# Performance work log

Hardware: AMD Instinct MI355X
Metric: run time of the kernel (lower is better)

Reference implementation:

```python
import jax, jax.numpy as jnp
import numpy as np

B, T, M, K = 8, 128, 8, 16
EMBED, HID = 64, 128
KR = K + 1
N = M * KR
NEG_SLOPE = 0.2


def build_edges(num_instruments, k_with_root):
    edges = []
    Kr = k_with_root
    for m in range(num_instruments):
        base = m * Kr
        root = base + (Kr - 1)
        for kp in range(Kr - 1):
            edges.append((base + kp, root))
            edges.append((root, base + kp))
    roots = [m * Kr + (Kr - 1) for m in range(num_instruments)]
    for i in range(len(roots)):
        for j in range(i + 1, len(roots)):
            edges.append((roots[i], roots[j]))
            edges.append((roots[j], roots[i]))
    e = np.asarray(edges, dtype=np.int32)
    return jnp.asarray(e[:, 0]), jnp.asarray(e[:, 1])


def setup_inputs() -> dict:
    key = jax.random.key(0)
    ks = jax.random.split(key, 12)
    feat = jax.random.uniform(ks[0], (B, T, M, K, 3), dtype=jnp.float32)
    sc = 0.05
    W1 = jax.random.normal(ks[1], (3, EMBED), jnp.float32) * sc
    b1 = jnp.zeros((EMBED,), jnp.float32)
    W2 = jax.random.normal(ks[2], (EMBED, EMBED), jnp.float32) * sc
    b2 = jnp.zeros((EMBED,), jnp.float32)
    W_ih = jax.random.normal(ks[3], (4 * HID, EMBED), jnp.float32) * sc
    W_hh = jax.random.normal(ks[4], (4 * HID, HID), jnp.float32) * sc
    b_ih = jnp.zeros((4 * HID,), jnp.float32)
    b_hh = jnp.zeros((4 * HID,), jnp.float32)
    Wg = jax.random.normal(ks[5], (HID, HID), jnp.float32) * sc
    a_src = jax.random.normal(ks[6], (HID,), jnp.float32) * sc
    a_dst = jax.random.normal(ks[7], (HID,), jnp.float32) * sc
    src, dst = build_edges(M, KR)
    return {"feat": feat, "W1": W1, "b1": b1, "W2": W2, "b2": b2,
            "W_ih": W_ih, "W_hh": W_hh, "b_ih": b_ih, "b_hh": b_hh,
            "Wg": Wg, "a_src": a_src, "a_dst": a_dst, "src": src, "dst": dst}


def reference(feat, W1, b1, W2, b2, W_ih, W_hh, b_ih, b_hh, Wg, a_src, a_dst, src, dst):
    # --- add_virtual_root: (B,T,M,K,3) -> (B,T,M,K+1,3) ---
    xy = feat[..., :2]
    vis = feat[..., 2] > 0.5
    w = vis[..., None].astype(feat.dtype)
    denom = jnp.clip(jnp.sum(w, axis=3, keepdims=True), 1.0, None)
    root_xy = jnp.sum(xy * w, axis=3, keepdims=True) / denom
    root_vis = jnp.any(vis, axis=3, keepdims=True).astype(feat.dtype)[..., None]
    root_feat = jnp.concatenate([root_xy, root_vis], axis=-1)
    featR = jnp.concatenate([feat, root_feat], axis=3)  # (B,T,M,KR,3)
    b, t, m, kr, _ = featR.shape
    n = m * kr
    # --- phi MLP ---
    v = jnp.maximum(featR @ W1 + b1, 0.0) @ W2 + b2  # (B,T,M,KR,E)
    v = v.reshape(b, t, n, -1)
    # --- LSTM over time, batch = B*N (torch gate order i,f,g,o) ---
    x = v.transpose(1, 0, 2, 3).reshape(t, b * n, -1)  # (T, B*N, E)
    hdim = W_hh.shape[1]
    h0 = jnp.zeros((b * n, hdim), feat.dtype)
    def step(carry, xt):
        h, c = carry
        z = xt @ W_ih.T + b_ih + h @ W_hh.T + b_hh
        i, f, g, o = jnp.split(z, 4, axis=-1)
        c = jax.nn.sigmoid(f) * c + jax.nn.sigmoid(i) * jnp.tanh(g)
        h = jax.nn.sigmoid(o) * jnp.tanh(c)
        return (h, c), h
    _, hs = jax.lax.scan(step, (h0, h0), x)  # (T, B*N, H)
    r = hs.reshape(t, b, n, hdim).transpose(1, 0, 2, 3)  # (B,T,N,H)
    # --- GAT applied to all timesteps at once (fixed edge_index) ---
    h = r @ Wg                           # (B,T,N,H)
    s_src = h @ a_src                    # (B,T,N)
    s_dst = h @ a_dst
    e = s_src[:, :, src] + s_dst[:, :, dst]           # (B,T,E)
    e = jnp.where(e > 0, e, NEG_SLOPE * e)            # LeakyReLU(0.2)
    eT = e.transpose(2, 0, 1)                          # (E,B,T)
    mmax = jax.ops.segment_max(eT, dst, num_segments=n)  # (N,B,T)
    ex = jnp.exp(eT - mmax[dst])
    den = jax.ops.segment_sum(ex, dst, num_segments=n)   # (N,B,T)
    alpha = ex / den[dst]                               # (E,B,T)
    hT = h.transpose(2, 0, 1, 3)                        # (N,B,T,H)
    agg = jax.ops.segment_sum(alpha[..., None] * hT[src], dst, num_segments=n)
    rhat = jax.nn.elu(agg).transpose(1, 2, 0, 3)        # (B,T,N,H)
    return (r, rhat)
```

## Files before the change

### kernel.cpp

```cpp
#include <hip/hip_runtime.h>

#define TB 128
#define BB 8
#define MM 8
#define KP 16
#define KR 17
#define NN 136
#define EMB 64
#define HID 128
#define G4 512
#define BN 1088
#define NEG_SLOPE 0.2f

typedef _Float16 h4 __attribute__((ext_vector_type(4)));
typedef _Float16 h8 __attribute__((ext_vector_type(8)));
typedef float    f4v __attribute__((ext_vector_type(4)));

__device__ __forceinline__ float sigf(float x) { return 1.0f/(1.0f + __expf(-x)); }
__device__ __forceinline__ float tanhf_fast(float x) {
  x = fminf(fmaxf(x, -15.0f), 15.0f);
  float e = __expf(2.0f*x);
  return (e - 1.0f)/(e + 1.0f);
}
__device__ __forceinline__ void bar_lds() {
  asm volatile("s_waitcnt lgkmcnt(0)\n\ts_barrier" ::: "memory");
}

__global__ __launch_bounds__(256) void k1_mlp(
    const float* __restrict__ feat, const float* __restrict__ W1,
    const float* __restrict__ b1, const float* __restrict__ W2,
    const float* __restrict__ b2, float* __restrict__ x)
{
  __shared__ float fl[MM*KP*3];
  __shared__ float fR[NN][3];
  __shared__ float hidl[NN][EMB];
  const int bt = blockIdx.x;
  const int b = bt >> 7;
  const int t = bt & 127;
  const int tid = threadIdx.x;

  const float* fp = feat + (size_t)bt * (MM*KP*3);
  for (int i = tid; i < MM*KP*3; i += 256) fl[i] = fp[i];
  __syncthreads();

  if (tid < NN) {
    int n = tid, m = n / KR, kk = n - m*KR;
    if (kk < KP) {
      fR[n][0] = fl[(m*KP+kk)*3+0];
      fR[n][1] = fl[(m*KP+kk)*3+1];
      fR[n][2] = fl[(m*KP+kk)*3+2];
    } else {
      float sx = 0.f, sy = 0.f, sw = 0.f;
      for (int k = 0; k < KP; ++k) {
        float vz = fl[(m*KP+k)*3+2];
        float w = (vz > 0.5f) ? 1.0f : 0.0f;
        sx += fl[(m*KP+k)*3+0]*w;
        sy += fl[(m*KP+k)*3+1]*w;
        sw += w;
      }
      float dn = fmaxf(sw, 1.0f);
      fR[n][0] = sx/dn; fR[n][1] = sy/dn; fR[n][2] = (sw > 0.f) ? 1.f : 0.f;
    }
  }
  __syncthreads();

  const int p = tid & 31, e0 = p*2, nb = tid >> 5;
  float w10a = W1[e0],   w11a = W1[EMB+e0],   w12a = W1[2*EMB+e0],   b1a = b1[e0];
  float w10b = W1[e0+1], w11b = W1[EMB+e0+1], w12b = W1[2*EMB+e0+1], b1b = b1[e0+1];
  for (int ni = 0; ni < 17; ++ni) {
    int n = nb*17 + ni;
    float xx = fR[n][0], yy = fR[n][1], zz = fR[n][2];
    float va = fmaf(xx,w10a, fmaf(yy,w11a, fmaf(zz,w12a, b1a)));
    float vb = fmaf(xx,w10b, fmaf(yy,w11b, fmaf(zz,w12b, b1b)));
    *(float2*)&hidl[n][e0] = make_float2(fmaxf(va,0.f), fmaxf(vb,0.f));
  }
  float2 w2c[EMB];
  #pragma unroll
  for (int j = 0; j < EMB; ++j) w2c[j] = *(const float2*)&W2[(size_t)j*EMB + e0];
  float b2a = b2[e0], b2b = b2[e0+1];
  __syncthreads();

  float* xo = x + ((size_t)t*BN + (size_t)b*NN)*EMB + e0;
  for (int ni = 0; ni < 17; ++ni) {
    int n = nb*17 + ni;
    float aa = b2a, ab = b2b;
    const float4* h4p = (const float4*)hidl[n];
    #pragma unroll
    for (int j4 = 0; j4 < 16; ++j4) {
      float4 hv = h4p[j4];
      aa = fmaf(hv.x, w2c[4*j4+0].x, aa); ab = fmaf(hv.x, w2c[4*j4+0].y, ab);
      aa = fmaf(hv.y, w2c[4*j4+1].x, aa); ab = fmaf(hv.y, w2c[4*j4+1].y, ab);
      aa = fmaf(hv.z, w2c[4*j4+2].x, aa); ab = fmaf(hv.z, w2c[4*j4+2].y, ab);
      aa = fmaf(hv.w, w2c[4*j4+3].x, aa); ab = fmaf(hv.w, w2c[4*j4+3].y, ab);
    }
    *(float2*)&xo[(size_t)n*EMB] = make_float2(aa, ab);
  }
}

__global__ __launch_bounds__(512, 2) void k2_lstm(
    const float* __restrict__ x, const float* __restrict__ W_ih,
    const float* __restrict__ W_hh, const float* __restrict__ b_ih,
    const float* __restrict__ b_hh, float* __restrict__ r)
{
  __shared__ h8  Bh8[6*64];
  __shared__ h8  Bl8[6*64];
  __shared__ f4v zlds[32*64];
  const int tid = threadIdx.x;
  const int w   = tid >> 6;
  const int l   = tid & 63;
  const int lr  = l & 15;
  const int lg  = l >> 4;
  const int s0  = blockIdx.x * 16;

  h8 A[4][6];
  #pragma unroll
  for (int m = 0; m < 4; ++m) {
    int row = 64*w + 16*m + lr;
    const float* wih = W_ih + (size_t)row*64;
    const float* whh = W_hh + (size_t)row*128;
    #pragma unroll
    for (int kt = 0; kt < 6; ++kt) {
      int k = kt*32 + lg*8;
      float4 wv0 = (k < 64) ? *(const float4*)(wih + k)
                            : *(const float4*)(whh + (k - 64));
      float4 wv1 = (k+4 < 64) ? *(const float4*)(wih + k + 4)
                              : *(const float4*)(whh + (k + 4 - 64));
      A[m][kt] = h8{(_Float16)wv0.x,(_Float16)wv0.y,(_Float16)wv0.z,(_Float16)wv0.w,
                    (_Float16)wv1.x,(_Float16)wv1.y,(_Float16)wv1.z,(_Float16)wv1.w};
    }
  }
  #pragma unroll
  for (int m = 0; m < 4; ++m)
    #pragma unroll
    for (int kt = 0; kt < 6; ++kt)
      asm volatile("" : "+v"(A[m][kt]));

  f4v biasC[4];
  #pragma unroll
  for (int m = 0; m < 4; ++m)
    #pragma unroll
    for (int q = 0; q < 4; ++q) {
      int row = 64*w + 16*m + lg*4 + q;
      biasC[m][q] = b_ih[row] + b_hh[row];
    }

  const int j0 = 16*w + 4*lg;
  const int l2    = lr + 16*(2*(w&1) + (lg>>1));
  const int halfB = lg & 1;
  const int hIdx  = (2 + (w>>1))*64 + l2;
  const int xIdx  = (w>>1)*64 + l2;

  const int qq = s0 + lr;
  const int b  = qq / NN, n = qq - b*NN;
  float* rp0 = r + (((size_t)b*TB)*NN + n)*HID + j0;
  const size_t rstep = (size_t)NN*HID;

  {
    h4 z0 = h4{(_Float16)0.f,(_Float16)0.f,(_Float16)0.f,(_Float16)0.f};
    ((h4*)Bh8)[256 + tid] = z0;
    ((h4*)Bl8)[256 + tid] = z0;
    if (w < 4) {
      float4 xv = *(const float4*)(x + ((size_t)(s0 + lr))*EMB + 16*w + 4*lg);
      h4 xh = h4{(_Float16)xv.x,(_Float16)xv.y,(_Float16)xv.z,(_Float16)xv.w};
      h4 xl = h4{(_Float16)(xv.x-(float)xh[0]),(_Float16)(xv.y-(float)xh[1]),
                 (_Float16)(xv.z-(float)xh[2]),(_Float16)(xv.w-(float)xh[3])};
      ((h4*)&Bh8[xIdx])[halfB] = xh;
      ((h4*)&Bl8[xIdx])[halfB] = xl;
    }
  }
  __syncthreads();

  float c0=0.f, c1=0.f, c2=0.f, c3=0.f;

  for (int t = 0; t < TB; ++t) {
    float4 xpre = make_float4(0.f,0.f,0.f,0.f);
    if (w < 4) {
      int tp = (t+1 < TB) ? t+1 : t;
      xpre = *(const float4*)(x + ((size_t)tp*BN + s0 + lr)*EMB + 16*w + 4*lg);
    }

    f4v C[4] = {biasC[0], biasC[1], biasC[2], biasC[3]};
    #pragma unroll
    for (int kt = 0; kt < 6; ++kt) {
      h8 bh = Bh8[kt*64 + l];
      h8 bl = Bl8[kt*64 + l];
      #pragma unroll
      for (int m = 0; m < 4; ++m)
        C[m] = __builtin_amdgcn_mfma_f32_16x16x32_f16(A[m][kt], bh, C[m], 0, 0, 0);
      #pragma unroll
      for (int m = 0; m < 4; ++m)
        C[m] = __builtin_amdgcn_mfma_f32_16x16x32_f16(A[m][kt], bl, C[m], 0, 0, 0);
    }
    #pragma unroll
    for (int m = 0; m < 4; ++m) zlds[(4*w + m)*64 + l] = C[m];
    bar_lds();

    f4v zi = zlds[(0*8 + w)*64 + l];
    f4v zf = zlds[(1*8 + w)*64 + l];
    f4v zg = zlds[(2*8 + w)*64 + l];
    f4v zo = zlds[(3*8 + w)*64 + l];
    float h0,h1,h2,h3;
    { float cc = sigf(zf[0])*c0 + sigf(zi[0])*tanhf_fast(zg[0]); h0 = sigf(zo[0])*tanhf_fast(cc); c0 = cc; }
    { float cc = sigf(zf[1])*c1 + sigf(zi[1])*tanhf_fast(zg[1]); h1 = sigf(zo[1])*tanhf_fast(cc); c1 = cc; }
    { float cc = sigf(zf[2])*c2 + sigf(zi[2])*tanhf_fast(zg[2]); h2 = sigf(zo[2])*tanhf_fast(cc); c2 = cc; }
    { float cc = sigf(zf[3])*c3 + sigf(zi[3])*tanhf_fast(zg[3]); h3 = sigf(zo[3])*tanhf_fast(cc); c3 = cc; }
    *(float4*)(rp0 + (size_t)t*rstep) = make_float4(h0,h1,h2,h3);
    h4 hh = h4{(_Float16)h0,(_Float16)h1,(_Float16)h2,(_Float16)h3};
    h4 hl = h4{(_Float16)(h0-(float)hh[0]),(_Float16)(h1-(float)hh[1]),
               (_Float16)(h2-(float)hh[2]),(_Float16)(h3-(float)hh[3])};
    ((h4*)&Bh8[hIdx])[halfB] = hh;
    ((h4*)&Bl8[hIdx])[halfB] = hl;
    if (w < 4) {
      h4 xh = h4{(_Float16)xpre.x,(_Float16)xpre.y,(_Float16)xpre.z,(_Float16)xpre.w};
      h4 xl = h4{(_Float16)(xpre.x-(float)xh[0]),(_Float16)(xpre.y-(float)xh[1]),
                 (_Float16)(xpre.z-(float)xh[2]),(_Float16)(xpre.w-(float)xh[3])};
      ((h4*)&Bh8[xIdx])[halfB] = xh;
      ((h4*)&Bl8[xIdx])[halfB] = xl;
    }
    bar_lds();
  }
}

__global__ __launch_bounds__(256) void k3_gat(
    const float* __restrict__ r, const float* __restrict__ Wg,
    const float* __restrict__ a_src, const float* __restrict__ a_dst,
    float* __restrict__ rhat)
{
  __shared__ float rl[NN*132];
  __shared__ float waS[HID], waD[HID];
  __shared__ float ssrc[NN], sdst[NN];
  __shared__ float alpha[MM][24];
  __shared__ float aggR[MM][HID];
  __shared__ float v16[HID*20];
  __shared__ float h2[16][HID];
  const int bt = blockIdx.x;
  const int tid = threadIdx.x;
  const float* rb = r + (size_t)bt*NN*HID;

  {
    const float4* rb4 = (const float4*)rb;
    for (int i = tid; i < NN*32; i += 256) {
      int n = i >> 5, k4 = i & 31;
      *(float4*)&rl[n*132 + k4*4] = rb4[i];
    }
  }
  {
    int half = tid >> 7, j = tid & 127;
    const float* av = half ? a_dst : a_src;
    float acc = 0.f;
    for (int k = 0; k < HID; ++k) acc = fmaf(Wg[(size_t)k*HID + j], av[k], acc);
    if (half) waD[j] = acc; else waS[j] = acc;
  }
  __syncthreads();
  for (int job = tid; job < 2*NN; job += 256) {
    int n = job >> 1, which = job & 1;
    const float4* rn = (const float4*)&rl[n*132];
    const float4* wa = (const float4*)(which ? waD : waS);
    float acc = 0.f;
    #pragma unroll
    for (int i = 0; i < 32; ++i) {
      float4 a4 = rn[i], b4 = wa[i];
      acc = fmaf(a4.x,b4.x, fmaf(a4.y,b4.y, fmaf(a4.z,b4.z, fmaf(a4.w,b4.w, acc))));
    }
    if (which) sdst[n] = acc; else ssrc[n] = acc;
  }
  __syncthreads();
  if (tid < MM) {
    int m = tid;
    float sd = sdst[m*KR + KP];
    float ev[23]; float mx = -1e30f;
    #pragma unroll
    for (int k = 0; k < 23; ++k) {
      int srcn;
      if (k < KP) srcn = m*KR + k;
      else { int rr = k - KP; rr += (rr >= m) ? 1 : 0; srcn = rr*KR + KP; }
      float e = ssrc[srcn] + sd;
      e = (e > 0.f) ? e : NEG_SLOPE*e;
      ev[k] = e; mx = fmaxf(mx, e);
    }
    float den = 0.f;
    #pragma unroll
    for (int k = 0; k < 23; ++k) { float ex = __expf(ev[k]-mx); ev[k] = ex; den += ex; }
    float inv = 1.f/den;
    #pragma unroll
    for (int k = 0; k < 23; ++k) alpha[m][k] = ev[k]*inv;
  }
  __syncthreads();
  {
    int m = tid >> 5, jq = (tid & 31)*4;
    float4 acc = make_float4(0.f,0.f,0.f,0.f);
    #pragma unroll
    for (int k = 0; k < 23; ++k) {
      int srcn;
      if (k < KP) srcn = m*KR + k;
      else { int rr = k - KP; rr += (rr >= m) ? 1 : 0; srcn = rr*KR + KP; }
      float al = alpha[m][k];
      float4 hv = *(const float4*)&rl[srcn*132 + jq];
      acc.x = fmaf(al, hv.x, acc.x); acc.y = fmaf(al, hv.y, acc.y);
      acc.z = fmaf(al, hv.z, acc.z); acc.w = fmaf(al, hv.w, acc.w);
    }
    *(float4*)&aggR[m][jq] = acc;
  }
  __syncthreads();
  for (int idx = tid; idx < 16*HID; idx += 256) {
    int k = idx & 127, row = idx >> 7;
    float v = (row < 8) ? rl[(row*KR + KP)*132 + k] : aggR[row-8][k];
    v16[k*20 + row] = v;
  }
  __syncthreads();
  {
    int half = tid >> 7, j = tid & 127;
    float acc[8] = {0.f,0.f,0.f,0.f,0.f,0.f,0.f,0.f};
    const float* wgp = Wg + j;
    #pragma unroll 4
    for (int k = 0; k < HID; ++k) {
      float wv = wgp[(size_t)k*HID];
      const float4* vv = (const float4*)&v16[k*20 + half*8];
      float4 va = vv[0], vb = vv[1];
      acc[0] = fmaf(va.x, wv, acc[0]); acc[1] = fmaf(va.y, wv, acc[1]);
      acc[2] = fmaf(va.z, wv, acc[2]); acc[3] = fmaf(va.w, wv, acc[3]);
      acc[4] = fmaf(vb.x, wv, acc[4]); acc[5] = fmaf(vb.y, wv, acc[5]);
      acc[6] = fmaf(vb.z, wv, acc[6]); acc[7] = fmaf(vb.w, wv, acc[7]);
    }
    #pragma unroll
    for (int q = 0; q < 8; ++q) h2[half*8 + q][j] = acc[q];
  }
  __syncthreads();
  {
    int j = tid & 127, half = tid >> 7;
    float* out = rhat + (size_t)bt*NN*HID + j;
    for (int ni = 0; ni < 68; ++ni) {
      int n = half*68 + ni;
      int m = n / KR, kk = n - m*KR;
      float v = (kk < KP) ? h2[m][j] : h2[8+m][j];
      v = (v > 0.f) ? v : (__expf(v) - 1.f);
      out[(size_t)n*HID] = v;
    }
  }
}

extern "C" void kernel_launch(void* const* d_in, const int* in_sizes, int n_in,
                              void* d_out, int out_size, void* d_ws, size_t ws_size,
                              hipStream_t stream) {
  (void)in_sizes; (void)n_in; (void)out_size; (void)ws_size;
  const float* feat  = (const float*)d_in[0];
  const float* W1    = (const float*)d_in[1];
  const float* b1    = (const float*)d_in[2];
  const float* W2    = (const float*)d_in[3];
  const float* b2    = (const float*)d_in[4];
  const float* W_ih  = (const float*)d_in[5];
  const float* W_hh  = (const float*)d_in[6];
  const float* b_ih  = (const float*)d_in[7];
  const float* b_hh  = (const float*)d_in[8];
  const float* Wg    = (const float*)d_in[9];
  const float* a_src = (const float*)d_in[10];
  const float* a_dst = (const float*)d_in[11];

  float* x    = (float*)d_ws;
  float* r    = (float*)d_out;
  float* rhat = r + (size_t)BB*TB*NN*HID;

  k1_mlp<<<BB*TB, 256, 0, stream>>>(feat, W1, b1, W2, b2, x);
  k2_lstm<<<68, 512, 0, stream>>>(x, W_ih, W_hh, b_ih, b_hh, r);
  k3_gat<<<BB*TB, 256, 0, stream>>>(r, Wg, a_src, a_dst, rhat);
}
```

Measured before the change: 607.7 us.

## Remap LSTM gate rows per wave and precompute next-step input projection

Each wave now owns matching rows of all four gates (i,f,g,o) for its 16 hidden units. The z staging buffer in LDS and one of the two barriers per timestep are gone, since the gate math reads the MFMA accumulators directly. The B operand buffers are double-buffered, and the x-part of the next step's gate preactivation (kt 0-1) is computed after the current step's gate math. That takes the input-projection MFMAs off the serial recurrent critical path. The cost is extra accumulator registers, a prologue step, and a prefetch of x two steps ahead.

```diff
diff --git a/kernel.cpp b/kernel.cpp
--- a/kernel.cpp
+++ b/kernel.cpp
@@ -102,9 +102,8 @@
     const float* __restrict__ W_hh, const float* __restrict__ b_ih,
     const float* __restrict__ b_hh, float* __restrict__ r)
 {
-  __shared__ h8  Bh8[6*64];
-  __shared__ h8  Bl8[6*64];
-  __shared__ f4v zlds[32*64];
+  __shared__ h8  Bh8[2][6*64];
+  __shared__ h8  Bl8[2][6*64];
   const int tid = threadIdx.x;
   const int w   = tid >> 6;
   const int l   = tid & 63;
@@ -114,8 +113,8 @@
 
   h8 A[4][6];
   #pragma unroll
-  for (int m = 0; m < 4; ++m) {
-    int row = 64*w + 16*m + lr;
+  for (int g = 0; g < 4; ++g) {
+    int row = 128*g + 16*w + lr;
     const float* wih = W_ih + (size_t)row*64;
     const float* whh = W_hh + (size_t)row*128;
     #pragma unroll
@@ -125,30 +124,30 @@
                             : *(const float4*)(whh + (k - 64));
       float4 wv1 = (k+4 < 64) ? *(const float4*)(wih + k + 4)
                               : *(const float4*)(whh + (k + 4 - 64));
-      A[m][kt] = h8{(_Float16)wv0.x,(_Float16)wv0.y,(_Float16)wv0.z,(_Float16)wv0.w,
+      A[g][kt] = h8{(_Float16)wv0.x,(_Float16)wv0.y,(_Float16)wv0.z,(_Float16)wv0.w,
                     (_Float16)wv1.x,(_Float16)wv1.y,(_Float16)wv1.z,(_Float16)wv1.w};
     }
   }
   #pragma unroll
-  for (int m = 0; m < 4; ++m)
+  for (int g = 0; g < 4; ++g)
     #pragma unroll
     for (int kt = 0; kt < 6; ++kt)
-      asm volatile("" : "+v"(A[m][kt]));
+      asm volatile("" : "+v"(A[g][kt]));
 
   f4v biasC[4];
   #pragma unroll
-  for (int m = 0; m < 4; ++m)
+  for (int g = 0; g < 4; ++g)
     #pragma unroll
     for (int q = 0; q < 4; ++q) {
-      int row = 64*w + 16*m + lg*4 + q;
-      biasC[m][q] = b_ih[row] + b_hh[row];
-    }
-
-  const int j0 = 16*w + 4*lg;
+      int row = 128*g + 16*w + 4*lg + q;
+      biasC[g][q] = b_ih[row] + b_hh[row];
+    }
+
+  const int j0    = 16*w + 4*lg;
   const int l2    = lr + 16*(2*(w&1) + (lg>>1));
   const int halfB = lg & 1;
-  const int hIdx  = (2 + (w>>1))*64 + l2;
-  const int xIdx  = (w>>1)*64 + l2;
+  const int hEnt  = (2 + (w>>1))*64 + l2;
+  const int xEnt  = (w>>1)*64 + l2;
 
   const int qq = s0 + lr;
   const int b  = qq / NN, n = qq - b*NN;
@@ -157,48 +156,69 @@
 
   {
     h4 z0 = h4{(_Float16)0.f,(_Float16)0.f,(_Float16)0.f,(_Float16)0.f};
-    ((h4*)Bh8)[256 + tid] = z0;
-    ((h4*)Bl8)[256 + tid] = z0;
+    ((h4*)&Bh8[0][0])[256 + tid] = z0;
+    ((h4*)&Bl8[0][0])[256 + tid] = z0;
     if (w < 4) {
       float4 xv = *(const float4*)(x + ((size_t)(s0 + lr))*EMB + 16*w + 4*lg);
       h4 xh = h4{(_Float16)xv.x,(_Float16)xv.y,(_Float16)xv.z,(_Float16)xv.w};
       h4 xl = h4{(_Float16)(xv.x-(float)xh[0]),(_Float16)(xv.y-(float)xh[1]),
                  (_Float16)(xv.z-(float)xh[2]),(_Float16)(xv.w-(float)xh[3])};
-      ((h4*)&Bh8[xIdx])[halfB] = xh;
-      ((h4*)&Bl8[xIdx])[halfB] = xl;
-    }
+      ((h4*)&Bh8[0][xEnt])[halfB] = xh;
+      ((h4*)&Bl8[0][xEnt])[halfB] = xl;
+    }
+  }
+  __syncthreads();
+
+  f4v Cp[4] = {biasC[0], biasC[1], biasC[2], biasC[3]};
+  #pragma unroll
+  for (int kt = 0; kt < 2; ++kt) {
+    h8 bh = Bh8[0][kt*64 + l];
+    h8 bl = Bl8[0][kt*64 + l];
+    #pragma unroll
+    for (int g = 0; g < 4; ++g)
+      Cp[g] = __builtin_amdgcn_mfma_f32_16x16x32_f16(A[g][kt], bh, Cp[g], 0, 0, 0);
+    #pragma unroll
+    for (int g = 0; g < 4; ++g)
+      Cp[g] = __builtin_amdgcn_mfma_f32_16x16x32_f16(A[g][kt], bl, Cp[g], 0, 0, 0);
+  }
+  __syncthreads();
+  if (w < 4) {
+    float4 xv = *(const float4*)(x + ((size_t)BN + s0 + lr)*EMB + 16*w + 4*lg);
+    h4 xh = h4{(_Float16)xv.x,(_Float16)xv.y,(_Float16)xv.z,(_Float16)xv.w};
+    h4 xl = h4{(_Float16)(xv.x-(float)xh[0]),(_Float16)(xv.y-(float)xh[1]),
+               (_Float16)(xv.z-(float)xh[2]),(_Float16)(xv.w-(float)xh[3])};
+    ((h4*)&Bh8[0][xEnt])[halfB] = xh;
+    ((h4*)&Bl8[0][xEnt])[halfB] = xl;
   }
   __syncthreads();
 
   float c0=0.f, c1=0.f, c2=0.f, c3=0.f;
 
   for (int t = 0; t < TB; ++t) {
+    const int p = t & 1;
     float4 xpre = make_float4(0.f,0.f,0.f,0.f);
     if (w < 4) {
-      int tp = (t+1 < TB) ? t+1 : t;
+      int tp = (t+2 < TB) ? t+2 : TB-1;
       xpre = *(const float4*)(x + ((size_t)tp*BN + s0 + lr)*EMB + 16*w + 4*lg);
     }
 
-    f4v C[4] = {biasC[0], biasC[1], biasC[2], biasC[3]};
-    #pragma unroll
-    for (int kt = 0; kt < 6; ++kt) {
-      h8 bh = Bh8[kt*64 + l];
-      h8 bl = Bl8[kt*64 + l];
+    f4v C[4] = {Cp[0], Cp[1], Cp[2], Cp[3]};
+    #pragma unroll
+    for (int kt = 2; kt < 6; ++kt) {
+      h8 bh = Bh8[p][kt*64 + l];
+      h8 bl = Bl8[p][kt*64 + l];
       #pragma unroll
-      for (int m = 0; m < 4; ++m)
-        C[m] = __builtin_amdgcn_mfma_f32_16x16x32_f16(A[m][kt], bh, C[m], 0, 0, 0);
+      for (int g = 0; g < 4; ++g)
+        C[g] = __builtin_amdgcn_mfma_f32_16x16x32_f16(A[g][kt], bh, C[g], 0, 0, 0);
       #pragma unroll
-      for (int m = 0; m < 4; ++m)
-        C[m] = __builtin_amdgcn_mfma_f32_16x16x32_f16(A[m][kt], bl, C[m], 0, 0, 0);
-    }
-    #pragma unroll
-    for (int m = 0; m < 4; ++m) zlds[(4*w + m)*64 + l] = C[m];
-    bar_lds();
-
-    f4v zi = zlds[(0*8 + w)*64 + l];
-    f4v zf = zlds[(1*8 + w)*64 + l];
-    f4v zg = zlds[(2*8 + w)*64 + l];
-    f4v zo = zlds[(3*8 + w)*64 + l];
+      for (int g = 0; g < 4; ++g)
+        C[g] = __builtin_amdgcn_mfma_f32_16x16x32_f16(A[g][kt], bl, C[g], 0, 0, 0);
+    }
+
+    h8 xbh0 = Bh8[p][0*64 + l], xbl0 = Bl8[p][0*64 + l];
+    h8 xbh1 = Bh8[p][1*64 + l], xbl1 = Bl8[p][1*64 + l];
+
+    f4v zi = C[0], zf = C[1], zg = C[2], zo = C[3];
     float h0,h1,h2,h3;
     { float cc = sigf(zf[0])*c0 + sigf(zi[0])*tanhf_fast(zg[0]); h0 = sigf(zo[0])*tanhf_fast(cc); c0 = cc; }
     { float cc = sigf(zf[1])*c1 + sigf(zi[1])*tanhf_fast(zg[1]); h1 = sigf(zo[1])*tanhf_fast(cc); c1 = cc; }
@@ -208,14 +228,29 @@
     h4 hh = h4{(_Float16)h0,(_Float16)h1,(_Float16)h2,(_Float16)h3};
     h4 hl = h4{(_Float16)(h0-(float)hh[0]),(_Float16)(h1-(float)hh[1]),
                (_Float16)(h2-(float)hh[2]),(_Float16)(h3-(float)hh[3])};
-    ((h4*)&Bh8[hIdx])[halfB] = hh;
-    ((h4*)&Bl8[hIdx])[halfB] = hl;
+    ((h4*)&Bh8[1-p][hEnt])[halfB] = hh;
+    ((h4*)&Bl8[1-p][hEnt])[halfB] = hl;
+
+    Cp[0] = biasC[0]; Cp[1] = biasC[1]; Cp[2] = biasC[2]; Cp[3] = biasC[3];
+    #pragma unroll
+    for (int g = 0; g < 4; ++g)
+      Cp[g] = __builtin_amdgcn_mfma_f32_16x16x32_f16(A[g][0], xbh0, Cp[g], 0, 0, 0);
+    #pragma unroll
+    for (int g = 0; g < 4; ++g)
+      Cp[g] = __builtin_amdgcn_mfma_f32_16x16x32_f16(A[g][0], xbl0, Cp[g], 0, 0, 0);
+    #pragma unroll
+    for (int g = 0; g < 4; ++g)
+      Cp[g] = __builtin_amdgcn_mfma_f32_16x16x32_f16(A[g][1], xbh1, Cp[g], 0, 0, 0);
+    #pragma unroll
+    for (int g = 0; g < 4; ++g)
+      Cp[g] = __builtin_amdgcn_mfma_f32_16x16x32_f16(A[g][1], xbl1, Cp[g], 0, 0, 0);
+
     if (w < 4) {
       h4 xh = h4{(_Float16)xpre.x,(_Float16)xpre.y,(_Float16)xpre.z,(_Float16)xpre.w};
       h4 xl = h4{(_Float16)(xpre.x-(float)xh[0]),(_Float16)(xpre.y-(float)xh[1]),
                  (_Float16)(xpre.z-(float)xh[2]),(_Float16)(xpre.w-(float)xh[3])};
-      ((h4*)&Bh8[xIdx])[halfB] = xh;
-      ((h4*)&Bl8[xIdx])[halfB] = xl;
+      ((h4*)&Bh8[1-p][xEnt])[halfB] = xh;
+      ((h4*)&Bl8[1-p][xEnt])[halfB] = xl;
     }
     bar_lds();
   }
```

Result: faster. 555.7 us (-8.6%).
